# Performance work log

Measured on AMD Instinct MI355X. Metric: run time of the kernel, lower is better.

The kernel has to match this reference:

```python
import jax, jax.numpy as jnp
import numpy as np

N_NODES = 100000
N_GRAPHS = 64

def gcn_conv(x, edge_index, W, b, num_nodes):
    # PyG GCNConv: x' = D^-1/2 (A + I) D^-1/2 (x W) + b
    h = x @ W  # [N, out]
    row, col = edge_index[0], edge_index[1]
    loops = jnp.arange(num_nodes, dtype=row.dtype)
    src = jnp.concatenate([row, loops])  # message source (x_j)
    dst = jnp.concatenate([col, loops])  # aggregation target
    deg = jax.ops.segment_sum(jnp.ones_like(src, dtype=h.dtype), dst,
                              num_segments=num_nodes)
    dinv = jnp.where(deg > 0, jax.lax.rsqrt(deg), 0.0)
    norm = dinv[src] * dinv[dst]  # [E+N]
    msgs = h[src] * norm[:, None]  # gather-transform
    out = jax.ops.segment_sum(msgs, dst, num_segments=num_nodes)  # scatter
    return out + b

def global_mean_pool(x, batch, num_graphs):
    sums = jax.ops.segment_sum(x, batch, num_segments=num_graphs)
    cnts = jax.ops.segment_sum(jnp.ones((x.shape[0],), x.dtype), batch,
                               num_segments=num_graphs)
    return sums / jnp.maximum(cnts, 1.0)[:, None]

def setup_inputs() -> dict:
    key = jax.random.key(0)
    ks = jax.random.split(key, 12)
    d_in, d_hid, d_mid, d_out = 128, 128, 20, 10
    n_edges = 1600000
    x = jax.random.normal(ks[0], (N_NODES, d_in), dtype=jnp.float32)
    edge_index = jax.random.randint(ks[1], (2, n_edges), 0, N_NODES, dtype=jnp.int64)
    batch = jnp.sort(jax.random.randint(ks[2], (N_NODES,), 0, N_GRAPHS, dtype=jnp.int64))
    def glorot(k, fan_in, fan_out):
        s = (6.0 / (fan_in + fan_out)) ** 0.5
        return jax.random.uniform(k, (fan_in, fan_out), jnp.float32, -s, s)
    return {
        "x": x, "edge_index": edge_index, "batch": batch,
        "W1": glorot(ks[3], d_in, d_hid), "b1": jnp.zeros((d_hid,), jnp.float32),
        "W2": glorot(ks[4], d_hid, d_hid), "b2": jnp.zeros((d_hid,), jnp.float32),
        "fc1_W": glorot(ks[5], d_hid, d_mid), "fc1_b": jnp.zeros((d_mid,), jnp.float32),
        "fc2_W": glorot(ks[6], d_mid, d_out), "fc2_b": jnp.zeros((d_out,), jnp.float32),
    }

def reference(x, edge_index, batch, W1, b1, W2, b2, fc1_W, fc1_b, fc2_W, fc2_b):
    # eval mode: dropout is identity
    h = gcn_conv(x, edge_index, W1, b1, N_NODES)
    h = jax.nn.elu(h)
    h = gcn_conv(h, edge_index, W2, b2, N_NODES)
    g = global_mean_pool(h, batch, N_GRAPHS)  # [G, hidden]
    g = jax.nn.relu(g @ fc1_W + fc1_b)
    g = g @ fc2_W + fc2_b
    return jax.nn.log_softmax(g, axis=1)
```

## Files before the change

kernel.cpp:

```cpp
#include <hip/hip_runtime.h>
#include <math.h>

#define DH 128
#define BCAP 16384

typedef __bf16 bf8_t __attribute__((ext_vector_type(8)));
typedef short short8 __attribute__((ext_vector_type(8)));
typedef float f4_t __attribute__((ext_vector_type(4)));
typedef float f2_t __attribute__((ext_vector_type(2)));

__device__ inline unsigned short f2b(float f) {
    unsigned int u = __builtin_bit_cast(unsigned int, f);
    u = u + 0x7fffu + ((u >> 16) & 1u);
    return (unsigned short)(u >> 16);
}
__device__ inline float b2f(unsigned short h) {
    return __builtin_bit_cast(float, (unsigned int)h << 16);
}

__global__ __launch_bounds__(256) void k_bucket(const int* __restrict__ row,
                                                const int* __restrict__ col,
                                                int E, int nbuck, int chunk,
                                                unsigned int* __restrict__ pairs,
                                                int* __restrict__ bcur) {
    __shared__ int lcnt[256];
    __shared__ int lbase[256];
    __shared__ unsigned int srec[8192];
    int t = threadIdx.x;
    int e0 = blockIdx.x * chunk;
    int e1 = min(e0 + chunk, E);
    lcnt[t] = 0;
    __syncthreads();
    for (int i = e0 + t; i < e1; i += 256) {
        int d = col[i];
        int b = d >> 9;
        int slot = atomicAdd(&lcnt[b], 1);
        srec[i - e0] = ((unsigned int)b << 22) | ((unsigned int)(d & 511) << 13)
                     | (unsigned int)slot;
    }
    __syncthreads();
    if (t < nbuck) {
        int c = lcnt[t];
        lbase[t] = (c > 0) ? atomicAdd(&bcur[t * 16], c) : 0;
    }
    __syncthreads();
    for (int i = e0 + t; i < e1; i += 256) {
        unsigned int r = srec[i - e0];
        int b = r >> 22;
        unsigned int dl = (r >> 13) & 511u;
        int slot = (int)(r & 8191u);
        int g = lbase[b] + slot;
        if (g < BCAP)
            pairs[(size_t)b * BCAP + g] = ((unsigned int)row[i] << 9) | dl;
    }
}

__global__ __launch_bounds__(256) void k_build(const unsigned int* __restrict__ pairs,
                                               const int* __restrict__ bcur,
                                               int nbuck, int N,
                                               int* __restrict__ off,
                                               float* __restrict__ dinv,
                                               int* __restrict__ csr) {
    __shared__ int sb[256];
    __shared__ int cnt2[512];
    __shared__ int excl[512];
    __shared__ int curi[512];
    __shared__ int stmp[256];
    int b = blockIdx.x, t = threadIdx.x;
    sb[t] = (t < nbuck) ? min(bcur[t * 16], BCAP) : 0;
    __syncthreads();
    for (int d = 1; d < 256; d <<= 1) {
        int v = (t >= d) ? sb[t - d] : 0;
        __syncthreads();
        sb[t] += v;
        __syncthreads();
    }
    int base = (b == 0) ? 0 : sb[b - 1];
    int cnt = sb[b] - base;
    int node0 = b << 9;
    int nodes = min(512, N - node0);
    cnt2[t] = 0; cnt2[t + 256] = 0;
    __syncthreads();
    const unsigned int* pp = pairs + (size_t)b * BCAP;
    for (int i = t; i < cnt; i += 256)
        atomicAdd(&cnt2[pp[i] & 511u], 1);
    __syncthreads();
    stmp[t] = cnt2[2 * t] + cnt2[2 * t + 1];
    __syncthreads();
    for (int d = 1; d < 256; d <<= 1) {
        int v = (t >= d) ? stmp[t - d] : 0;
        __syncthreads();
        stmp[t] += v;
        __syncthreads();
    }
    int pre = (t == 0) ? 0 : stmp[t - 1];
    excl[2 * t] = pre;
    excl[2 * t + 1] = pre + cnt2[2 * t];
    __syncthreads();
    if (t < nodes) {
        off[node0 + t] = base + excl[t];
        dinv[node0 + t] = rsqrtf((float)(cnt2[t] + 1));
    }
    int t2 = t + 256;
    if (t2 < nodes) {
        off[node0 + t2] = base + excl[t2];
        dinv[node0 + t2] = rsqrtf((float)(cnt2[t2] + 1));
    }
    if (t == 0) off[node0 + nodes] = base + cnt;
    curi[t] = excl[t]; curi[t + 256] = excl[t + 256];
    __syncthreads();
    for (int i = t; i < cnt; i += 256) {
        unsigned int p = pp[i];
        int d = (int)(p & 511u);
        int slot = atomicAdd(&curi[d], 1);
        csr[base + slot] = (int)(p >> 9);
    }
}

__global__ void k_prepW(const float* __restrict__ W1, const float* __restrict__ W2,
                        unsigned short* __restrict__ Wt1, unsigned short* __restrict__ Wt2) {
    int t = blockIdx.x * blockDim.x + threadIdx.x;
    const float* W = (t < 16384) ? W1 : W2;
    unsigned short* Wt = (t < 16384) ? Wt1 : Wt2;
    int v = t & 16383;
    int k = v >> 7, n = v & 127;
    Wt[n * DH + k] = f2b(W[k * DH + n]);
}

__global__ __launch_bounds__(256) void k_gemm_mfma(const void* __restrict__ Xin, int x_is_bf16,
                                                   const unsigned short* __restrict__ Wt,
                                                   const float* __restrict__ dinv,
                                                   unsigned char* __restrict__ Y, int nrows) {
    __shared__ unsigned short Xs[64 * 136];
    __shared__ unsigned short Ws[128 * 136];
    int t = threadIdx.x;
    int row0 = blockIdx.x * 64;

    for (int v = t; v < 128 * 32; v += 256) {
        int n = v >> 5, kq = v & 31;
        ushort4 w = ((const ushort4*)Wt)[v];
        *(ushort4*)&Ws[n * 136 + kq * 4] = w;
    }
    if (x_is_bf16) {
        const unsigned short* X = (const unsigned short*)Xin;
        for (int v = t; v < 64 * 32; v += 256) {
            int r = v >> 5, cq = v & 31;
            int gr = row0 + r;
            ushort4 h;
            if (gr < nrows) h = ((const ushort4*)X)[(size_t)gr * 32 + cq];
            else { h.x = 0; h.y = 0; h.z = 0; h.w = 0; }
            *(ushort4*)&Xs[r * 136 + cq * 4] = h;
        }
    } else {
        const float* X = (const float*)Xin;
        for (int v = t; v < 64 * 32; v += 256) {
            int r = v >> 5, cq = v & 31;
            int gr = row0 + r;
            ushort4 h;
            if (gr < nrows) {
                float4 xv = ((const float4*)X)[(size_t)gr * 32 + cq];
                h.x = f2b(xv.x); h.y = f2b(xv.y); h.z = f2b(xv.z); h.w = f2b(xv.w);
            } else { h.x = 0; h.y = 0; h.z = 0; h.w = 0; }
            *(ushort4*)&Xs[r * 136 + cq * 4] = h;
        }
    }
    __syncthreads();

    int w = t >> 6;
    int lane = t & 63;
    int quad = lane >> 4;
    int l16 = lane & 15;
    int rw = w * 16;

    f4_t acc[8];
#pragma unroll
    for (int j = 0; j < 8; j++) acc[j] = (f4_t){0.f, 0.f, 0.f, 0.f};

#pragma unroll
    for (int kk = 0; kk < 4; kk++) {
        int k0 = kk * 32;
        bf8_t a = __builtin_bit_cast(bf8_t,
            *(const short8*)&Xs[(rw + l16) * 136 + k0 + quad * 8]);
#pragma unroll
        for (int j = 0; j < 8; j++) {
            bf8_t b = __builtin_bit_cast(bf8_t,
                *(const short8*)&Ws[(j * 16 + l16) * 136 + k0 + quad * 8]);
            acc[j] = __builtin_amdgcn_mfma_f32_16x16x32_bf16(a, b, acc[j], 0, 0, 0);
        }
    }

#pragma unroll
    for (int reg = 0; reg < 4; reg++) {
        int r = row0 + rw + quad * 4 + reg;
        if (r < nrows) {
            float dv = dinv[r];
            float v0 = acc[0][reg] * dv, v1 = acc[1][reg] * dv;
            float v2 = acc[2][reg] * dv, v3 = acc[3][reg] * dv;
            float v4 = acc[4][reg] * dv, v5 = acc[5][reg] * dv;
            float v6 = acc[6][reg] * dv, v7 = acc[7][reg] * dv;
            int d0 = __builtin_amdgcn_cvt_pk_fp8_f32(v0, v1, 0, false);
            d0 = __builtin_amdgcn_cvt_pk_fp8_f32(v2, v3, d0, true);
            int d1 = __builtin_amdgcn_cvt_pk_fp8_f32(v4, v5, 0, false);
            d1 = __builtin_amdgcn_cvt_pk_fp8_f32(v6, v7, d1, true);
            *(uint2*)&Y[(size_t)r * DH + l16 * 8] = make_uint2((unsigned)d0, (unsigned)d1);
        }
    }
}

__global__ __launch_bounds__(256) void k_agg(const unsigned char* __restrict__ T,
                                             unsigned short* __restrict__ Out,
                                             const float* __restrict__ dinv,
                                             const int* __restrict__ off,
                                             const int* __restrict__ csr,
                                             const float* __restrict__ bias,
                                             int elu, int N) {
    int t = threadIdx.x;
    int d = blockIdx.x * 4 + (t >> 6);
    if (d >= N) return;
    int lane = t & 63;
    int half = lane >> 5;
    int l5 = lane & 31;

    int s0 = off[d];
    int deg = off[d + 1] - s0;

    int jl = (lane < deg) ? csr[s0 + lane] : 0;

    float a0 = 0.f, a1 = 0.f, a2 = 0.f, a3 = 0.f;

    unsigned int vs = half ? 0u
        : *(const unsigned int*)(T + (size_t)d * DH + (l5 << 2));
    {
        f2_t lo = __builtin_amdgcn_cvt_pk_f32_fp8(vs, false);
        f2_t hi = __builtin_amdgcn_cvt_pk_f32_fp8(vs, true);
        a0 += lo[0]; a1 += lo[1]; a2 += hi[0]; a3 += hi[1];
    }

    int dcl = min(deg, 64);
    int k = half;
    for (; k + 2 < dcl; k += 4) {
        int j0 = __shfl(jl, k);
        int j1 = __shfl(jl, k + 2);
        unsigned int v0 = *(const unsigned int*)(T + (size_t)j0 * DH + (l5 << 2));
        unsigned int v1 = *(const unsigned int*)(T + (size_t)j1 * DH + (l5 << 2));
        f2_t lo0 = __builtin_amdgcn_cvt_pk_f32_fp8(v0, false);
        f2_t hi0 = __builtin_amdgcn_cvt_pk_f32_fp8(v0, true);
        f2_t lo1 = __builtin_amdgcn_cvt_pk_f32_fp8(v1, false);
        f2_t hi1 = __builtin_amdgcn_cvt_pk_f32_fp8(v1, true);
        a0 += lo0[0] + lo1[0];
        a1 += lo0[1] + lo1[1];
        a2 += hi0[0] + hi1[0];
        a3 += hi0[1] + hi1[1];
    }
    if (k < dcl) {
        int j0 = __shfl(jl, k);
        unsigned int v0 = *(const unsigned int*)(T + (size_t)j0 * DH + (l5 << 2));
        f2_t lo0 = __builtin_amdgcn_cvt_pk_f32_fp8(v0, false);
        f2_t hi0 = __builtin_amdgcn_cvt_pk_f32_fp8(v0, true);
        a0 += lo0[0]; a1 += lo0[1]; a2 += hi0[0]; a3 += hi0[1];
    }
    for (int q = 64 + half; q < deg; q += 2) {
        int j = csr[s0 + q];
        unsigned int v0 = *(const unsigned int*)(T + (size_t)j * DH + (l5 << 2));
        f2_t lo0 = __builtin_amdgcn_cvt_pk_f32_fp8(v0, false);
        f2_t hi0 = __builtin_amdgcn_cvt_pk_f32_fp8(v0, true);
        a0 += lo0[0]; a1 += lo0[1]; a2 += hi0[0]; a3 += hi0[1];
    }

    a0 += __shfl_xor(a0, 32);
    a1 += __shfl_xor(a1, 32);
    a2 += __shfl_xor(a2, 32);
    a3 += __shfl_xor(a3, 32);

    if (half == 0) {
        float dv = dinv[d];
        int base = ((l5 & 1) << 6) | (l5 >> 1);
        float o0 = a0 * dv + bias[base];
        float o1 = a1 * dv + bias[base + 16];
        float o2 = a2 * dv + bias[base + 32];
        float o3 = a3 * dv + bias[base + 48];
        if (elu) {
            o0 = o0 > 0.f ? o0 : expm1f(o0);
            o1 = o1 > 0.f ? o1 : expm1f(o1);
            o2 = o2 > 0.f ? o2 : expm1f(o2);
            o3 = o3 > 0.f ? o3 : expm1f(o3);
        }
        unsigned short* orow = Out + (size_t)d * DH;
        orow[base]      = f2b(o0);
        orow[base + 16] = f2b(o1);
        orow[base + 32] = f2b(o2);
        orow[base + 48] = f2b(o3);
    }
}

__global__ __launch_bounds__(256) void k_pool(const unsigned int* __restrict__ H32,
                                              const int* __restrict__ batch,
                                              float* __restrict__ Gsum,
                                              int* __restrict__ cnts, int N) {
    int g = blockIdx.x;
    int p = blockIdx.y;
    int t = threadIdx.x;
    int lane = t & 63;
    int rg = t >> 6;
    int lo = 0, hi = N;
    while (lo < hi) { int m = (lo + hi) >> 1; if (batch[m] < g) lo = m + 1; else hi = m; }
    int s = lo;
    hi = N;
    while (lo < hi) { int m = (lo + hi) >> 1; if (batch[m] < g + 1) lo = m + 1; else hi = m; }
    int e = lo;
    int len = e - s;
    int parts = (int)gridDim.y;
    int chunk = (len + parts - 1) / parts;
    int i0 = s + p * chunk;
    int i1 = min(i0 + chunk, e);
    float a0 = 0.f, a1 = 0.f;
    for (int i = i0 + rg; i < i1; i += 4) {
        unsigned int v = H32[(size_t)i * 64 + lane];
        a0 += b2f((unsigned short)(v & 0xffffu));
        a1 += b2f((unsigned short)(v >> 16));
    }
    __shared__ float ps[4][DH];
    ps[rg][lane * 2] = a0;
    ps[rg][lane * 2 + 1] = a1;
    __syncthreads();
    if (t < DH) {
        float v = ps[0][t] + ps[1][t] + ps[2][t] + ps[3][t];
        atomicAdd(&Gsum[g * DH + t], v);
    }
    if (p == 0 && t == 0) cnts[g] = len;
}

__global__ __launch_bounds__(64) void k_head(const float* __restrict__ Gsum,
                                             const int* __restrict__ cnts,
                                             const float* __restrict__ W1,
                                             const float* __restrict__ b1,
                                             const float* __restrict__ W2,
                                             const float* __restrict__ b2,
                                             float* __restrict__ out) {
    int g = blockIdx.x;
    int t = threadIdx.x;
    __shared__ float gv[DH];
    __shared__ float mid[20];
    __shared__ float o[10];
    float inv = 1.f / fmaxf((float)cnts[g], 1.f);
    for (int i = t; i < DH; i += 64) gv[i] = Gsum[g * DH + i] * inv;
    __syncthreads();
    if (t < 20) {
        float a = b1[t];
        for (int k = 0; k < DH; k++) a += gv[k] * W1[k * 20 + t];
        mid[t] = fmaxf(a, 0.f);
    }
    __syncthreads();
    if (t < 10) {
        float a = b2[t];
        for (int k = 0; k < 20; k++) a += mid[k] * W2[k * 10 + t];
        o[t] = a;
    }
    __syncthreads();
    if (t == 0) {
        float m = -1e30f;
        for (int j = 0; j < 10; j++) m = fmaxf(m, o[j]);
        float ssum = 0.f;
        for (int j = 0; j < 10; j++) ssum += expf(o[j] - m);
        float l = logf(ssum);
        for (int j = 0; j < 10; j++) out[g * 10 + j] = o[j] - m - l;
    }
}

extern "C" void kernel_launch(void* const* d_in, const int* in_sizes, int n_in,
                              void* d_out, int out_size, void* d_ws, size_t ws_size,
                              hipStream_t stream) {
    const float* x    = (const float*)d_in[0];
    const int*   ei   = (const int*)d_in[1];
    const int*   batch= (const int*)d_in[2];
    const float* W1   = (const float*)d_in[3];
    const float* b1   = (const float*)d_in[4];
    const float* W2   = (const float*)d_in[5];
    const float* b2   = (const float*)d_in[6];
    const float* fc1W = (const float*)d_in[7];
    const float* fc1b = (const float*)d_in[8];
    const float* fc2W = (const float*)d_in[9];
    const float* fc2b = (const float*)d_in[10];
    float* out = (float*)d_out;

    int N = in_sizes[0] / DH;
    int E = in_sizes[1] / 2;
    int G = out_size / 10;

    char* p = (char*)d_ws;
    auto alloc = [&](size_t bytes) {
        char* r = p;
        p += (bytes + 255) & ~(size_t)255;
        return r;
    };
    unsigned char*  t8 = (unsigned char*)alloc((size_t)N * DH);
    unsigned short* a1 = (unsigned short*)alloc((size_t)N * DH * 2);
    int*   csr  = (int*)alloc((size_t)E * 4);
    int*   off  = (int*)alloc((size_t)(N + 1) * 4);
    float* dinv = (float*)alloc((size_t)N * 4);
    int nbuck = (N + 511) >> 9;
    unsigned int* pairs = (unsigned int*)alloc((size_t)nbuck * BCAP * 4);
    unsigned short* Wt1 = (unsigned short*)alloc(DH * DH * 2);
    unsigned short* Wt2 = (unsigned short*)alloc(DH * DH * 2);
    float* Gsum = (float*)alloc((size_t)G * DH * 4);
    int*   bcur = (int*)alloc(256 * 16 * 4);
    int*   cnts = (int*)alloc((size_t)G * 4);

    const int* row = ei;
    const int* col = ei + E;

    (void)hipMemsetAsync(Gsum, 0, (size_t)G * DH * 4 + 256 * 16 * 4, stream);

    const int chunk = 8192;
    int ablocks = (E + chunk - 1) / chunk;
    k_bucket<<<ablocks, 256, 0, stream>>>(row, col, E, nbuck, chunk, pairs, bcur);
    k_build<<<nbuck, 256, 0, stream>>>(pairs, bcur, nbuck, N, off, dinv, csr);
    k_prepW<<<128, 256, 0, stream>>>(W1, W2, Wt1, Wt2);

    int gblocks = (N + 63) / 64;
    int nblocks4 = (N + 3) / 4;
    k_gemm_mfma<<<gblocks, 256, 0, stream>>>(x, 0, Wt1, dinv, t8, N);
    k_agg<<<nblocks4, 256, 0, stream>>>(t8, a1, dinv, off, csr, b1, 1, N);
    k_gemm_mfma<<<gblocks, 256, 0, stream>>>(a1, 1, Wt2, dinv, t8, N);
    k_agg<<<nblocks4, 256, 0, stream>>>(t8, a1, dinv, off, csr, b2, 0, N);

    dim3 pg(G, 32);
    k_pool<<<pg, 256, 0, stream>>>((const unsigned int*)a1, batch, Gsum, cnts, N);
    k_head<<<G, 64, 0, stream>>>(Gsum, cnts, fc1W, fc1b, fc2W, fc2b, out);
}
```

Before: 329.4 us.

## Aggregate 16 nodes per block with shared-memory CSR staging and permuted output layout

The aggregation kernel now handles 16 destination nodes per block, four per wavefront in sequence. It stages the block's offsets and up to 768 neighbor indices in shared memory and unrolls the gather loop four-wide for more loads in flight. Output columns are written in a permuted order as one vectorized 8-byte store instead of four scattered 2-byte stores. The permutation is undone by permuting the rows of W2 in prepW and the pooled features in the head. The cost is fewer blocks, sequential per-wave node processing and an added layout coupling across kernels.

```diff
diff --git a/kernel.cpp b/kernel.cpp
--- a/kernel.cpp
+++ b/kernel.cpp
@@ -120,11 +120,14 @@
 __global__ void k_prepW(const float* __restrict__ W1, const float* __restrict__ W2,
                         unsigned short* __restrict__ Wt1, unsigned short* __restrict__ Wt2) {
     int t = blockIdx.x * blockDim.x + threadIdx.x;
-    const float* W = (t < 16384) ? W1 : W2;
-    unsigned short* Wt = (t < 16384) ? Wt1 : Wt2;
     int v = t & 16383;
     int k = v >> 7, n = v & 127;
-    Wt[n * DH + k] = f2b(W[k * DH + n]);
+    if (t < 16384) {
+        Wt1[n * DH + k] = f2b(W1[k * DH + n]);
+    } else {
+        int p = ((k & 15) << 3) | (k >> 4);
+        Wt2[n * DH + p] = f2b(W2[k * DH + n]);
+    }
 }
 
 __global__ __launch_bounds__(256) void k_gemm_mfma(const void* __restrict__ Xin, int x_is_bf16,
@@ -214,82 +217,125 @@
                                              const int* __restrict__ csr,
                                              const float* __restrict__ bias,
                                              int elu, int N) {
+    __shared__ int ofs[17];
+    __shared__ int sidx[768];
     int t = threadIdx.x;
-    int d = blockIdx.x * 4 + (t >> 6);
-    if (d >= N) return;
+    int d0 = blockIdx.x * 16;
+    if (t < 17) ofs[t] = off[min(d0 + t, N)];
+    __syncthreads();
+    int s0 = ofs[0];
+    int cnt = ofs[16] - s0;
+    int scnt = min(cnt, 768);
+    for (int k = t; k < scnt; k += 256) sidx[k] = csr[s0 + k];
+    __syncthreads();
+
+    int w = t >> 6;
     int lane = t & 63;
     int half = lane >> 5;
     int l5 = lane & 31;
-
-    int s0 = off[d];
-    int deg = off[d + 1] - s0;
-
-    int jl = (lane < deg) ? csr[s0 + lane] : 0;
-
-    float a0 = 0.f, a1 = 0.f, a2 = 0.f, a3 = 0.f;
-
-    unsigned int vs = half ? 0u
-        : *(const unsigned int*)(T + (size_t)d * DH + (l5 << 2));
-    {
-        f2_t lo = __builtin_amdgcn_cvt_pk_f32_fp8(vs, false);
-        f2_t hi = __builtin_amdgcn_cvt_pk_f32_fp8(vs, true);
-        a0 += lo[0]; a1 += lo[1]; a2 += hi[0]; a3 += hi[1];
-    }
-
-    int dcl = min(deg, 64);
-    int k = half;
-    for (; k + 2 < dcl; k += 4) {
-        int j0 = __shfl(jl, k);
-        int j1 = __shfl(jl, k + 2);
-        unsigned int v0 = *(const unsigned int*)(T + (size_t)j0 * DH + (l5 << 2));
-        unsigned int v1 = *(const unsigned int*)(T + (size_t)j1 * DH + (l5 << 2));
-        f2_t lo0 = __builtin_amdgcn_cvt_pk_f32_fp8(v0, false);
-        f2_t hi0 = __builtin_amdgcn_cvt_pk_f32_fp8(v0, true);
-        f2_t lo1 = __builtin_amdgcn_cvt_pk_f32_fp8(v1, false);
-        f2_t hi1 = __builtin_amdgcn_cvt_pk_f32_fp8(v1, true);
-        a0 += lo0[0] + lo1[0];
-        a1 += lo0[1] + lo1[1];
-        a2 += hi0[0] + hi1[0];
-        a3 += hi0[1] + hi1[1];
-    }
-    if (k < dcl) {
-        int j0 = __shfl(jl, k);
-        unsigned int v0 = *(const unsigned int*)(T + (size_t)j0 * DH + (l5 << 2));
-        f2_t lo0 = __builtin_amdgcn_cvt_pk_f32_fp8(v0, false);
-        f2_t hi0 = __builtin_amdgcn_cvt_pk_f32_fp8(v0, true);
-        a0 += lo0[0]; a1 += lo0[1]; a2 += hi0[0]; a3 += hi0[1];
-    }
-    for (int q = 64 + half; q < deg; q += 2) {
-        int j = csr[s0 + q];
-        unsigned int v0 = *(const unsigned int*)(T + (size_t)j * DH + (l5 << 2));
-        f2_t lo0 = __builtin_amdgcn_cvt_pk_f32_fp8(v0, false);
-        f2_t hi0 = __builtin_amdgcn_cvt_pk_f32_fp8(v0, true);
-        a0 += lo0[0]; a1 += lo0[1]; a2 += hi0[0]; a3 += hi0[1];
-    }
-
-    a0 += __shfl_xor(a0, 32);
-    a1 += __shfl_xor(a1, 32);
-    a2 += __shfl_xor(a2, 32);
-    a3 += __shfl_xor(a3, 32);
-
-    if (half == 0) {
-        float dv = dinv[d];
-        int base = ((l5 & 1) << 6) | (l5 >> 1);
-        float o0 = a0 * dv + bias[base];
-        float o1 = a1 * dv + bias[base + 16];
-        float o2 = a2 * dv + bias[base + 32];
-        float o3 = a3 * dv + bias[base + 48];
-        if (elu) {
-            o0 = o0 > 0.f ? o0 : expm1f(o0);
-            o1 = o1 > 0.f ? o1 : expm1f(o1);
-            o2 = o2 > 0.f ? o2 : expm1f(o2);
-            o3 = o3 > 0.f ? o3 : expm1f(o3);
-        }
-        unsigned short* orow = Out + (size_t)d * DH;
-        orow[base]      = f2b(o0);
-        orow[base + 16] = f2b(o1);
-        orow[base + 32] = f2b(o2);
-        orow[base + 48] = f2b(o3);
+    const unsigned char* Tl = T + (l5 << 2);
+
+    for (int ni = 0; ni < 4; ni++) {
+        int nd = d0 + 4 * w + ni;
+        if (nd >= N) break;
+        int eL = ofs[4 * w + ni] - s0;
+        int eH = ofs[4 * w + ni + 1] - s0;
+        int deg = eH - eL;
+
+        float a0, a1, a2, a3;
+        {
+            unsigned int u = *(const unsigned int*)(Tl + ((size_t)nd << 7));
+            if (half) u = 0;
+            f2_t lo = __builtin_amdgcn_cvt_pk_f32_fp8(u, false);
+            f2_t hi = __builtin_amdgcn_cvt_pk_f32_fp8(u, true);
+            a0 = lo[0]; a1 = lo[1]; a2 = hi[0]; a3 = hi[1];
+        }
+
+        if (eH <= scnt) {
+            int base_e = eL + half;
+            int Pf = deg >> 1;
+            int P4 = Pf & ~3;
+            int i = 0;
+            for (; i < P4; i += 4) {
+                int ea = base_e + 2 * i;
+                int j0 = sidx[ea];
+                int j1 = sidx[ea + 2];
+                int j2 = sidx[ea + 4];
+                int j3 = sidx[ea + 6];
+                unsigned int u0 = *(const unsigned int*)(Tl + ((size_t)j0 << 7));
+                unsigned int u1 = *(const unsigned int*)(Tl + ((size_t)j1 << 7));
+                unsigned int u2 = *(const unsigned int*)(Tl + ((size_t)j2 << 7));
+                unsigned int u3 = *(const unsigned int*)(Tl + ((size_t)j3 << 7));
+                f2_t lo0 = __builtin_amdgcn_cvt_pk_f32_fp8(u0, false);
+                f2_t hi0 = __builtin_amdgcn_cvt_pk_f32_fp8(u0, true);
+                f2_t lo1 = __builtin_amdgcn_cvt_pk_f32_fp8(u1, false);
+                f2_t hi1 = __builtin_amdgcn_cvt_pk_f32_fp8(u1, true);
+                f2_t lo2 = __builtin_amdgcn_cvt_pk_f32_fp8(u2, false);
+                f2_t hi2 = __builtin_amdgcn_cvt_pk_f32_fp8(u2, true);
+                f2_t lo3 = __builtin_amdgcn_cvt_pk_f32_fp8(u3, false);
+                f2_t hi3 = __builtin_amdgcn_cvt_pk_f32_fp8(u3, true);
+                a0 += (lo0[0] + lo1[0]) + (lo2[0] + lo3[0]);
+                a1 += (lo0[1] + lo1[1]) + (lo2[1] + lo3[1]);
+                a2 += (hi0[0] + hi1[0]) + (hi2[0] + hi3[0]);
+                a3 += (hi0[1] + hi1[1]) + (hi2[1] + hi3[1]);
+            }
+            for (; i < Pf; i++) {
+                int j0 = sidx[base_e + 2 * i];
+                unsigned int u0 = *(const unsigned int*)(Tl + ((size_t)j0 << 7));
+                f2_t lo = __builtin_amdgcn_cvt_pk_f32_fp8(u0, false);
+                f2_t hi = __builtin_amdgcn_cvt_pk_f32_fp8(u0, true);
+                a0 += lo[0]; a1 += lo[1]; a2 += hi[0]; a3 += hi[1];
+            }
+            if (deg & 1) {
+                int j0 = sidx[eL + deg - 1];
+                unsigned int u0 = *(const unsigned int*)(Tl + ((size_t)j0 << 7));
+                if (half) u0 = 0;
+                f2_t lo = __builtin_amdgcn_cvt_pk_f32_fp8(u0, false);
+                f2_t hi = __builtin_amdgcn_cvt_pk_f32_fp8(u0, true);
+                a0 += lo[0]; a1 += lo[1]; a2 += hi[0]; a3 += hi[1];
+            }
+        } else {
+            int gb = s0 + eL + half;
+            int Pf = deg >> 1;
+            for (int i = 0; i < Pf; i++) {
+                int j0 = csr[gb + 2 * i];
+                unsigned int u0 = *(const unsigned int*)(Tl + ((size_t)j0 << 7));
+                f2_t lo = __builtin_amdgcn_cvt_pk_f32_fp8(u0, false);
+                f2_t hi = __builtin_amdgcn_cvt_pk_f32_fp8(u0, true);
+                a0 += lo[0]; a1 += lo[1]; a2 += hi[0]; a3 += hi[1];
+            }
+            if (deg & 1) {
+                int j0 = csr[s0 + eL + deg - 1];
+                unsigned int u0 = *(const unsigned int*)(Tl + ((size_t)j0 << 7));
+                if (half) u0 = 0;
+                f2_t lo = __builtin_amdgcn_cvt_pk_f32_fp8(u0, false);
+                f2_t hi = __builtin_amdgcn_cvt_pk_f32_fp8(u0, true);
+                a0 += lo[0]; a1 += lo[1]; a2 += hi[0]; a3 += hi[1];
+            }
+        }
+
+        a0 += __shfl_xor(a0, 32);
+        a1 += __shfl_xor(a1, 32);
+        a2 += __shfl_xor(a2, 32);
+        a3 += __shfl_xor(a3, 32);
+
+        if (!half) {
+            float dv = dinv[nd];
+            int c0 = ((l5 & 1) << 6) | (l5 >> 1);
+            float o0 = a0 * dv + bias[c0];
+            float o1 = a1 * dv + bias[c0 + 16];
+            float o2 = a2 * dv + bias[c0 + 32];
+            float o3 = a3 * dv + bias[c0 + 48];
+            if (elu) {
+                o0 = o0 > 0.f ? o0 : expm1f(o0);
+                o1 = o1 > 0.f ? o1 : expm1f(o1);
+                o2 = o2 > 0.f ? o2 : expm1f(o2);
+                o3 = o3 > 0.f ? o3 : expm1f(o3);
+            }
+            unsigned int p0 = (unsigned int)f2b(o0) | ((unsigned int)f2b(o1) << 16);
+            unsigned int p1 = (unsigned int)f2b(o2) | ((unsigned int)f2b(o3) << 16);
+            *(uint2*)&Out[(size_t)nd * DH + (l5 << 2)] = make_uint2(p0, p1);
+        }
     }
 }
 
@@ -343,7 +389,10 @@
     __shared__ float mid[20];
     __shared__ float o[10];
     float inv = 1.f / fmaxf((float)cnts[g], 1.f);
-    for (int i = t; i < DH; i += 64) gv[i] = Gsum[g * DH + i] * inv;
+    for (int i = t; i < DH; i += 64) {
+        int c = ((i & 7) << 4) | (i >> 3);
+        gv[c] = Gsum[g * DH + i] * inv;
+    }
     __syncthreads();
     if (t < 20) {
         float a = b1[t];
@@ -418,11 +467,11 @@
     k_prepW<<<128, 256, 0, stream>>>(W1, W2, Wt1, Wt2);
 
     int gblocks = (N + 63) / 64;
-    int nblocks4 = (N + 3) / 4;
+    int mblocks = (N + 15) / 16;
     k_gemm_mfma<<<gblocks, 256, 0, stream>>>(x, 0, Wt1, dinv, t8, N);
-    k_agg<<<nblocks4, 256, 0, stream>>>(t8, a1, dinv, off, csr, b1, 1, N);
+    k_agg<<<mblocks, 256, 0, stream>>>(t8, a1, dinv, off, csr, b1, 1, N);
     k_gemm_mfma<<<gblocks, 256, 0, stream>>>(a1, 1, Wt2, dinv, t8, N);
-    k_agg<<<nblocks4, 256, 0, stream>>>(t8, a1, dinv, off, csr, b2, 0, N);
+    k_agg<<<mblocks, 256, 0, stream>>>(t8, a1, dinv, off, csr, b2, 0, N);
 
     dim3 pg(G, 32);
     k_pool<<<pg, 256, 0, stream>>>((const unsigned int*)a1, batch, Gsum, cnts, N);
```

Measured after the change: 312.1 us. -5.2%, faster.
